# Kernel optimization log

Hardware: AMD Instinct MI355X
Metric: run time of the kernel (lower is better)

The kernel has to match this reference:

```python
import jax, jax.numpy as jnp
import numpy as np

D = 1024       # d_model
H = 16         # nhead
HD = D // H    # head_dim = 64
FF = 4096      # dim_feedforward
EPS = 1e-5


def layer_norm(x, gamma, beta, eps=EPS):
    mu = jnp.mean(x, axis=-1, keepdims=True)
    var = jnp.var(x, axis=-1, keepdims=True)
    return (x - mu) * jax.lax.rsqrt(var + eps) * gamma + beta


def setup_inputs() -> dict:
    key = jax.random.key(0)
    ks = jax.random.split(key, 12)
    rn = lambda k, shape, s=0.02: (jax.random.normal(k, shape, jnp.float32) * s)
    return {
        "src": jax.random.normal(ks[0], (4, 2048, D), jnp.float32),
        "Wqkv": rn(ks[1], (D, 3 * D)),          # qkv_proj weight (bias=False), stored (in,out)
        "Wout": rn(ks[2], (D, D)),              # out_proj weight (bias=False)
        "W1": rn(ks[3], (D, FF)),               # linear1
        "b1": jnp.zeros((FF,), jnp.float32),
        "W2": rn(ks[4], (FF, D)),               # linear2
        "b2": jnp.zeros((D,), jnp.float32),
        "g1": jnp.ones((D,), jnp.float32),      # norm1 weight
        "be1": jnp.zeros((D,), jnp.float32),    # norm1 bias
        "g2": jnp.ones((D,), jnp.float32),      # norm2 weight
        "be2": jnp.zeros((D,), jnp.float32),    # norm2 bias
    }


def reference(src, Wqkv, Wout, W1, b1, W2, b2, g1, be1, g2, be2):
    B, S, _ = src.shape
    # --- self attention (naive/MATH-backend SDPA, post-norm, eval: dropout=0) ---
    qkv = src @ Wqkv                                  # [B,S,3D]
    qkv = qkv.reshape(B, S, 3, H, HD)
    q = qkv[:, :, 0].transpose(0, 2, 1, 3)            # [B,H,S,HD]
    k = qkv[:, :, 1].transpose(0, 2, 1, 3)
    v = qkv[:, :, 2].transpose(0, 2, 1, 3)
    scores = jnp.einsum("bhqd,bhkd->bhqk", q, k) / np.float32(np.sqrt(HD))  # [B,H,S,S]
    attn = jax.nn.softmax(scores, axis=-1)
    ctx = jnp.einsum("bhqk,bhkd->bhqd", attn, v)      # [B,H,S,HD]
    ctx = ctx.transpose(0, 2, 1, 3).reshape(B, S, D)  # [B,S,D]
    attn_out = ctx @ Wout
    # residual + norm1
    x = layer_norm(src + attn_out, g1, be1)
    # --- FFN ---
    ff = jax.nn.relu(x @ W1 + b1) @ W2 + b2
    # residual + norm2
    return layer_norm(x + ff, g2, be2)
```

## Files before the change

### kernel.cpp

```cpp
#include <hip/hip_runtime.h>
#include <hip/hip_bf16.h>


typedef __attribute__((ext_vector_type(8))) short          short8;
typedef __attribute__((ext_vector_type(8))) unsigned short ushort8;
typedef __attribute__((ext_vector_type(4))) float          f32x4;
typedef __attribute__((ext_vector_type(2))) unsigned int   uivec2;

__device__ __forceinline__ unsigned short f2bf(float f) {
    union { float f; unsigned int u; } v; v.f = f;
    unsigned int u = v.u;
    unsigned int r = (u + 0x7fffu + ((u >> 16) & 1u)) >> 16;
    return (unsigned short)r;
}

__device__ __forceinline__ float bf2f(unsigned short u) {
    union { unsigned int u; float f; } v; v.u = ((unsigned int)u) << 16;
    return v.f;
}

__device__ __forceinline__ unsigned int pack_bf16_trunc(float lo, float hi) {
    union { float f; unsigned int u; } a, b; a.f = lo; b.f = hi;
    return __builtin_amdgcn_perm(b.u, a.u, 0x07060302u);
}

__device__ __forceinline__ void async_load16(const void* g, void* l) {
    __builtin_amdgcn_global_load_lds(
        (const __attribute__((address_space(1))) void*)(unsigned long long)g,
        (__attribute__((address_space(3))) void*)(unsigned long long)l,
        16, 0, 0);
}

__global__ __launch_bounds__(256) void cast_bf16_kernel(
    const float* __restrict__ x, unsigned short* __restrict__ y) {
    size_t i = ((size_t)blockIdx.x * 256 + threadIdx.x) * 4;
    float4 v = *(const float4*)(x + i);
    ushort4 o; o.x = f2bf(v.x); o.y = f2bf(v.y); o.z = f2bf(v.z); o.w = f2bf(v.w);
    *(ushort4*)(y + i) = o;
}

__global__ __launch_bounds__(256) void transpose_cast_kernel(
    const float* __restrict__ W, unsigned short* __restrict__ Wt, int K, int N) {
    __shared__ float tile[32][33];
    int n0 = blockIdx.x * 32, k0 = blockIdx.y * 32;
    int tx = threadIdx.x & 31, ty = threadIdx.x >> 5;
#pragma unroll
    for (int i = 0; i < 32; i += 8)
        tile[ty + i][tx] = W[(size_t)(k0 + ty + i) * N + n0 + tx];
    __syncthreads();
#pragma unroll
    for (int i = 0; i < 32; i += 8)
        Wt[(size_t)(n0 + ty + i) * K + k0 + tx] = f2bf(tile[tx][ty + i]);
}

template <int MODE>
__global__ __launch_bounds__(256) void gemm_bf16_kernel(
    const unsigned short* __restrict__ A, const unsigned short* __restrict__ Bt,
    int M, int N, int K, int Kstride,
    float* __restrict__ outF, unsigned short* __restrict__ outB,
    const float* __restrict__ bias,
    const float* __restrict__ resF, const unsigned short* __restrict__ resB,
    unsigned short* __restrict__ vtB) {
    __shared__ unsigned short As[2][128 * 32];
    __shared__ unsigned short Bs[2][128 * 32];

    const int t = threadIdx.x;
    const int m0 = blockIdx.x * 128, n0 = blockIdx.y * 128;
    const int koff = blockIdx.z * K;
    const int wid = t >> 6, lane = t & 63;
    const int wm = wid >> 1, wn = wid & 1;
    const int lr = lane & 15, quad = lane >> 4;

    const int srow = lane >> 2;
    const int sch  = ((lane & 3) ^ (srow & 3)) * 8;
    const unsigned short* Ag =
        A  + (size_t)(m0 + wid * 32 + srow) * Kstride + koff + sch;
    const unsigned short* Bg =
        Bt + (size_t)(n0 + wid * 32 + srow) * Kstride + koff + sch;
    const int wofs = (wid * 32) * 32;
    const size_t rstep = (size_t)16 * Kstride;

    const int axs = ((quad ^ (lr & 3))) * 8;
    f32x4 acc[4][4] = {};

    const int nK = K >> 5;
    async_load16(Ag,         &As[0][wofs]);
    async_load16(Ag + rstep, &As[0][wofs + 16 * 32]);
    async_load16(Bg,         &Bs[0][wofs]);
    async_load16(Bg + rstep, &Bs[0][wofs + 16 * 32]);

    for (int kt = 0; kt < nK; kt++) {
        const int cur = kt & 1, nxt = cur ^ 1;
        __syncthreads();
        if (kt + 1 < nK) {
            const int k1 = (kt + 1) * 32;
            async_load16(Ag + k1,         &As[nxt][wofs]);
            async_load16(Ag + k1 + rstep, &As[nxt][wofs + 16 * 32]);
            async_load16(Bg + k1,         &Bs[nxt][wofs]);
            async_load16(Bg + k1 + rstep, &Bs[nxt][wofs + 16 * 32]);
        }

        short8 af[4], bfr[4];
#pragma unroll
        for (int i = 0; i < 4; i++) {
            af[i]  = *(const short8*)&As[cur][(wm * 64 + i * 16 + lr) * 32 + axs];
            bfr[i] = *(const short8*)&Bs[cur][(wn * 64 + i * 16 + lr) * 32 + axs];
        }
#pragma unroll
        for (int mi = 0; mi < 4; mi++)
#pragma unroll
            for (int ni = 0; ni < 4; ni++)
                acc[mi][ni] = __builtin_amdgcn_mfma_f32_16x16x32_bf16(
                    af[mi], bfr[ni], acc[mi][ni], 0, 0, 0);
    }

    const float QSC = 0.18033688011112042f;
    float* pOut = (MODE == 5) ? outF + (size_t)blockIdx.z * M * N : outF;
#pragma unroll
    for (int mi = 0; mi < 4; mi++)
#pragma unroll
        for (int ni = 0; ni < 4; ni++) {
            const int col  = n0 + wn * 64 + ni * 16 + lr;
            const int row0 = m0 + wm * 64 + mi * 16 + quad * 4;
            if (MODE == 4 && col >= 2048) {
                int bb = row0 >> 11, ss = row0 & 2047, c = col - 2048;
                ushort4 ov;
                ov.x = f2bf(acc[mi][ni][0]); ov.y = f2bf(acc[mi][ni][1]);
                ov.z = f2bf(acc[mi][ni][2]); ov.w = f2bf(acc[mi][ni][3]);
                *(ushort4*)&vtB[((size_t)bb * 1024 + c) * 2048 + ss] = ov;
            } else {
#pragma unroll
                for (int r = 0; r < 4; r++) {
                    size_t idx = (size_t)(row0 + r) * N + col;
                    float v = acc[mi][ni][r];
                    if (MODE == 4) {
                        outB[idx] = f2bf(col < 1024 ? v * QSC : v);
                    } else if (MODE == 0) {
                        outB[idx] = f2bf(v);
                    } else if (MODE == 1) {
                        outF[idx] = v + resF[idx];
                    } else if (MODE == 2) {
                        v += bias[col];
                        outB[idx] = f2bf(v > 0.f ? v : 0.f);
                    } else if (MODE == 3) {
                        outF[idx] = v + bias[col] + bf2f(resB[idx]);
                    } else {
                        pOut[idx] = v;
                    }
                }
            }
        }
}

__global__ __launch_bounds__(256) void attention_kernel(
    const unsigned short* __restrict__ qkv, const unsigned short* __restrict__ Vt,
    unsigned short* __restrict__ ctx) {
    __shared__ unsigned short Kbuf[2][64 * 64];
    __shared__ unsigned short Vbuf[2][64 * 64];

    const int qt = blockIdx.x, h = blockIdx.y, b = blockIdx.z;
    const int t = threadIdx.x, wid = t >> 6, lane = t & 63;
    const int lr = lane & 15, quad = lane >> 4;
    const int q0 = qt * 64 + wid * 16;

    size_t qbase = ((size_t)(b * 2048 + q0 + lr)) * 3072 + h * 64;
    short8 qf0 = *(const short8*)(qkv + qbase + quad * 8);
    short8 qf1 = *(const short8*)(qkv + qbase + 32 + quad * 8);

    const int srow = wid * 8 + (lane >> 3);
    const int sch  = ((lane & 7) ^ (srow & 7)) * 8;
    const unsigned short* Kg =
        qkv + (size_t)b * 2048 * 3072 + 1024 + h * 64 + (size_t)srow * 3072 + sch;
    const unsigned short* Vg =
        Vt + ((size_t)b * 1024 + h * 64 + srow) * 2048 + sch;
    unsigned short* KsB = (unsigned short*)&Kbuf[0][(wid * 8) * 64];
    unsigned short* VsB = (unsigned short*)&Vbuf[0][(wid * 8) * 64];
    const int bufstep = 64 * 64;

    short8 ones;
#pragma unroll
    for (int i = 0; i < 8; i++) ones[i] = (short)0x3F80;

    f32x4 o[4] = {};
    f32x4 lacc = {};

#pragma unroll
    for (int half = 0; half < 2; half++) {
        async_load16(Kg + (size_t)(half * 32) * 3072, KsB + half * 32 * 64);
        async_load16(Vg + (size_t)(half * 32) * 2048, VsB + half * 32 * 64);
    }

    const int swz = lr & 7;

    for (int kt = 0; kt < 32; kt++) {
        const int cur = kt & 1, nxt = cur ^ 1;
        __syncthreads();
        if (kt + 1 < 32) {
#pragma unroll
            for (int half = 0; half < 2; half++) {
                async_load16(Kg + (size_t)((kt + 1) * 64 + half * 32) * 3072,
                             KsB + nxt * bufstep + half * 32 * 64);
                async_load16(Vg + (size_t)(half * 32) * 2048 + (kt + 1) * 64,
                             VsB + nxt * bufstep + half * 32 * 64);
            }
        }

        const unsigned short* Kc = &Kbuf[cur][0];
        const unsigned short* Vc = &Vbuf[cur][0];

        f32x4 s[4] = {};
#pragma unroll
        for (int nt = 0; nt < 4; nt++) {
            const unsigned short* krow = Kc + (nt * 16 + lr) * 64;
            short8 kf0 = *(const short8*)(krow + (quad ^ swz) * 8);
            short8 kf1 = *(const short8*)(krow + ((quad + 4) ^ swz) * 8);
            s[nt] = __builtin_amdgcn_mfma_f32_16x16x32_bf16(kf0, qf0, s[nt], 0, 0, 0);
            s[nt] = __builtin_amdgcn_mfma_f32_16x16x32_bf16(kf1, qf1, s[nt], 0, 0, 0);
        }

        unsigned int aw[4], bw[4];
#pragma unroll
        for (int nt = 0; nt < 4; nt++) {
            float p0 = __builtin_amdgcn_exp2f(s[nt][0]);
            float p1 = __builtin_amdgcn_exp2f(s[nt][1]);
            float p2 = __builtin_amdgcn_exp2f(s[nt][2]);
            float p3 = __builtin_amdgcn_exp2f(s[nt][3]);
            aw[nt] = pack_bf16_trunc(p0, p1);
            bw[nt] = pack_bf16_trunc(p2, p3);
        }

        uivec2 rA = __builtin_amdgcn_permlane32_swap(aw[0], aw[1], false, false);
        uivec2 sA = __builtin_amdgcn_permlane32_swap(aw[2], aw[3], false, false);
        uivec2 rB = __builtin_amdgcn_permlane32_swap(bw[0], bw[1], false, false);
        uivec2 sB = __builtin_amdgcn_permlane32_swap(bw[2], bw[3], false, false);
        uivec2 tA = __builtin_amdgcn_permlane16_swap(rA.x, rA.y, false, false);
        uivec2 uA = __builtin_amdgcn_permlane16_swap(sA.x, sA.y, false, false);
        uivec2 tB = __builtin_amdgcn_permlane16_swap(rB.x, rB.y, false, false);
        uivec2 uB = __builtin_amdgcn_permlane16_swap(sB.x, sB.y, false, false);

        union { unsigned int w[4]; short8 v; } P0, P1;
        P0.w[0] = tA.x; P0.w[1] = tB.x; P0.w[2] = tA.y; P0.w[3] = tB.y;
        P1.w[0] = uA.x; P1.w[1] = uB.x; P1.w[2] = uA.y; P1.w[3] = uB.y;
        short8 pf0 = P0.v;
        short8 pf1 = P1.v;

#pragma unroll
        for (int nt = 0; nt < 4; nt++) {
            const unsigned short* vrow = Vc + (nt * 16 + lr) * 64;
            short8 vf0 = *(const short8*)(vrow + (quad ^ swz) * 8);
            short8 vf1 = *(const short8*)(vrow + ((quad + 4) ^ swz) * 8);
            o[nt] = __builtin_amdgcn_mfma_f32_16x16x32_bf16(pf0, vf0, o[nt], 0, 0, 0);
            o[nt] = __builtin_amdgcn_mfma_f32_16x16x32_bf16(pf1, vf1, o[nt], 0, 0, 0);
        }
        lacc = __builtin_amdgcn_mfma_f32_16x16x32_bf16(pf0, ones, lacc, 0, 0, 0);
        lacc = __builtin_amdgcn_mfma_f32_16x16x32_bf16(pf1, ones, lacc, 0, 0, 0);
    }

#pragma unroll
    for (int r = 0; r < 4; r++) {
        float li = 1.f / lacc[r];
        int q = qt * 64 + wid * 16 + quad * 4 + r;
#pragma unroll
        for (int nt = 0; nt < 4; nt++)
            ctx[((size_t)(b * 2048 + q)) * 1024 + h * 64 + nt * 16 + lr] =
                f2bf(o[nt][r] * li);
    }
}

template <int OUTMODE>
__global__ __launch_bounds__(256) void layernorm_kernel(
    const float* __restrict__ x, const float* __restrict__ g,
    const float* __restrict__ be, float* __restrict__ yF,
    unsigned short* __restrict__ yB) {
    const int row = blockIdx.x, t = threadIdx.x;
    const float* xr = x + (size_t)row * 1024;
    float4 v = *(const float4*)(xr + t * 4);
    float s  = v.x + v.y + v.z + v.w;
    float sq = v.x * v.x + v.y * v.y + v.z * v.z + v.w * v.w;
#pragma unroll
    for (int d = 1; d < 64; d <<= 1) {
        s  += __shfl_xor(s, d, 64);
        sq += __shfl_xor(sq, d, 64);
    }
    __shared__ float sh[8];
    int wid = t >> 6, lane = t & 63;
    if (lane == 0) { sh[wid] = s; sh[4 + wid] = sq; }
    __syncthreads();
    s  = sh[0] + sh[1] + sh[2] + sh[3];
    sq = sh[4] + sh[5] + sh[6] + sh[7];
    float mu  = s * (1.f / 1024.f);
    float var = sq * (1.f / 1024.f) - mu * mu;
    float rstd = rsqrtf(var + 1e-5f);
    float4 gv = *(const float4*)(g + t * 4);
    float4 bv = *(const float4*)(be + t * 4);
    float4 y;
    y.x = (v.x - mu) * rstd * gv.x + bv.x;
    y.y = (v.y - mu) * rstd * gv.y + bv.y;
    y.z = (v.z - mu) * rstd * gv.z + bv.z;
    y.w = (v.w - mu) * rstd * gv.w + bv.w;
    if (OUTMODE == 0) {
        *(float4*)(yF + (size_t)row * 1024 + t * 4) = y;
    } else {
        ushort4 o;
        o.x = f2bf(y.x); o.y = f2bf(y.y); o.z = f2bf(y.z); o.w = f2bf(y.w);
        *(ushort4*)(yB + (size_t)row * 1024 + t * 4) = o;
    }
}

__global__ __launch_bounds__(256) void layernorm_sum2_kernel(
    const float* __restrict__ p0, const float* __restrict__ p1,
    const float* __restrict__ bias, const unsigned short* __restrict__ res,
    const float* __restrict__ g, const float* __restrict__ be,
    float* __restrict__ out) {
    const int row = blockIdx.x, t = threadIdx.x;
    const size_t base = (size_t)row * 1024 + t * 4;
    float4 a = *(const float4*)(p0 + base);
    float4 b = *(const float4*)(p1 + base);
    float4 bi = *(const float4*)(bias + t * 4);
    ushort4 rb = *(const ushort4*)(res + base);
    float4 v;
    v.x = a.x + b.x + bi.x + bf2f(rb.x);
    v.y = a.y + b.y + bi.y + bf2f(rb.y);
    v.z = a.z + b.z + bi.z + bf2f(rb.z);
    v.w = a.w + b.w + bi.w + bf2f(rb.w);
    float s  = v.x + v.y + v.z + v.w;
    float sq = v.x * v.x + v.y * v.y + v.z * v.z + v.w * v.w;
#pragma unroll
    for (int d = 1; d < 64; d <<= 1) {
        s  += __shfl_xor(s, d, 64);
        sq += __shfl_xor(sq, d, 64);
    }
    __shared__ float sh[8];
    int wid = t >> 6, lane = t & 63;
    if (lane == 0) { sh[wid] = s; sh[4 + wid] = sq; }
    __syncthreads();
    s  = sh[0] + sh[1] + sh[2] + sh[3];
    sq = sh[4] + sh[5] + sh[6] + sh[7];
    float mu  = s * (1.f / 1024.f);
    float var = sq * (1.f / 1024.f) - mu * mu;
    float rstd = rsqrtf(var + 1e-5f);
    float4 gv = *(const float4*)(g + t * 4);
    float4 bv = *(const float4*)(be + t * 4);
    float4 y;
    y.x = (v.x - mu) * rstd * gv.x + bv.x;
    y.y = (v.y - mu) * rstd * gv.y + bv.y;
    y.z = (v.z - mu) * rstd * gv.z + bv.z;
    y.w = (v.w - mu) * rstd * gv.w + bv.w;
    *(float4*)(out + base) = y;
}

extern "C" void kernel_launch(void* const* d_in, const int* in_sizes, int n_in,
                              void* d_out, int out_size, void* d_ws, size_t ws_size,
                              hipStream_t stream) {
    const float* src  = (const float*)d_in[0];
    const float* Wqkv = (const float*)d_in[1];
    const float* Wout = (const float*)d_in[2];
    const float* W1   = (const float*)d_in[3];
    const float* b1   = (const float*)d_in[4];
    const float* W2   = (const float*)d_in[5];
    const float* b2   = (const float*)d_in[6];
    const float* g1   = (const float*)d_in[7];
    const float* be1  = (const float*)d_in[8];
    const float* g2   = (const float*)d_in[9];
    const float* be2  = (const float*)d_in[10];
    float* out = (float*)d_out;

    const size_t NT = 8192;
    char* ws = (char*)d_ws;
    unsigned short* src_bf = (unsigned short*)ws; ws += NT * 1024 * 2;
    unsigned short* Wqkv_t = (unsigned short*)ws; ws += (size_t)3072 * 1024 * 2;
    unsigned short* Wout_t = (unsigned short*)ws; ws += (size_t)1024 * 1024 * 2;
    unsigned short* W1_t   = (unsigned short*)ws; ws += (size_t)4096 * 1024 * 2;
    unsigned short* W2_t   = (unsigned short*)ws; ws += (size_t)1024 * 4096 * 2;
    unsigned short* qkv_bf = (unsigned short*)ws; ws += NT * 3072 * 2;
    unsigned short* ctx_bf = (unsigned short*)ws; ws += NT * 1024 * 2;
    float*          x1     = (float*)ws;          ws += NT * 1024 * 4;
    unsigned short* y1_bf  = (unsigned short*)ws; ws += NT * 1024 * 2;
    unsigned short* h_bf   = (unsigned short*)ws; ws += NT * 4096 * 2;
    unsigned short* Vt = h_bf;
    float* part = (float*)qkv_bf;

    cast_bf16_kernel<<<8192, 256, 0, stream>>>(src, src_bf);
    transpose_cast_kernel<<<dim3(96, 32), 256, 0, stream>>>(Wqkv, Wqkv_t, 1024, 3072);
    transpose_cast_kernel<<<dim3(32, 32), 256, 0, stream>>>(Wout, Wout_t, 1024, 1024);
    transpose_cast_kernel<<<dim3(128, 32), 256, 0, stream>>>(W1, W1_t, 1024, 4096);
    transpose_cast_kernel<<<dim3(32, 128), 256, 0, stream>>>(W2, W2_t, 4096, 1024);

    gemm_bf16_kernel<4><<<dim3(64, 24), 256, 0, stream>>>(
        src_bf, Wqkv_t, 8192, 3072, 1024, 1024,
        nullptr, qkv_bf, nullptr, nullptr, nullptr, Vt);
    attention_kernel<<<dim3(32, 16, 4), 256, 0, stream>>>(qkv_bf, Vt, ctx_bf);
    gemm_bf16_kernel<1><<<dim3(64, 8), 256, 0, stream>>>(
        ctx_bf, Wout_t, 8192, 1024, 1024, 1024,
        x1, nullptr, nullptr, src, nullptr, nullptr);
    layernorm_kernel<1><<<8192, 256, 0, stream>>>(x1, g1, be1, nullptr, y1_bf);
    gemm_bf16_kernel<2><<<dim3(64, 32), 256, 0, stream>>>(
        y1_bf, W1_t, 8192, 4096, 1024, 1024,
        nullptr, h_bf, b1, nullptr, nullptr, nullptr);
    gemm_bf16_kernel<5><<<dim3(64, 8, 2), 256, 0, stream>>>(
        h_bf, W2_t, 8192, 1024, 2048, 4096,
        part, nullptr, nullptr, nullptr, nullptr, nullptr);
    layernorm_sum2_kernel<<<8192, 256, 0, stream>>>(
        part, part + NT * 1024, b2, y1_bf, g2, be2, out);
}
```

Before: 520.4 us.

## Add 256x256 tile GEMM kernel with 4-stage async LDS pipeline for QKV/FFN

Adds a new 512-thread GEMM kernel that computes 256x256 output tiles. It uses a 4-slot LDS ring fed by async global-to-LDS loads, with explicit barriers, waitcnt control and raised wave priority around the MFMA bursts so loads overlap compute. The QKV, FF1 and split-K FF2 GEMMs switch to this kernel, while the old 128-tile kernel keeps only the modes that other launches still use. Larger tiles raise data reuse per loaded byte, but they cost 128KB of LDS per block and give fewer blocks, which can leave a partial wave on 256 CUs (for example 384 blocks for QKV).

After: 543.3 us. 4.4% more time.

```diff
diff --git a/kernel.cpp b/kernel.cpp
--- a/kernel.cpp
+++ b/kernel.cpp
@@ -114,14 +114,143 @@
                     af[mi], bfr[ni], acc[mi][ni], 0, 0, 0);
     }
 
-    const float QSC = 0.18033688011112042f;
-    float* pOut = (MODE == 5) ? outF + (size_t)blockIdx.z * M * N : outF;
 #pragma unroll
     for (int mi = 0; mi < 4; mi++)
 #pragma unroll
         for (int ni = 0; ni < 4; ni++) {
             const int col  = n0 + wn * 64 + ni * 16 + lr;
             const int row0 = m0 + wm * 64 + mi * 16 + quad * 4;
+#pragma unroll
+            for (int r = 0; r < 4; r++) {
+                size_t idx = (size_t)(row0 + r) * N + col;
+                float v = acc[mi][ni][r];
+                if (MODE == 0) {
+                    outB[idx] = f2bf(v);
+                } else if (MODE == 1) {
+                    outF[idx] = v + resF[idx];
+                }
+            }
+        }
+}
+
+#define GBAR() do { __builtin_amdgcn_sched_barrier(0); \
+                    __builtin_amdgcn_s_barrier();      \
+                    __builtin_amdgcn_sched_barrier(0); } while (0)
+
+template <int MODE>
+__global__ __launch_bounds__(512, 2) void gemm256_bf16_kernel(
+    const unsigned short* __restrict__ A, const unsigned short* __restrict__ Bt,
+    int M, int N, int K, int Kstride,
+    float* __restrict__ outF, unsigned short* __restrict__ outB,
+    const float* __restrict__ bias,
+    const float* __restrict__ resF, const unsigned short* __restrict__ resB,
+    unsigned short* __restrict__ vtB) {
+    __shared__ unsigned short Alds[4][256 * 32];
+    __shared__ unsigned short Blds[4][256 * 32];
+
+    const int t = threadIdx.x;
+    const int wid = t >> 6, lane = t & 63;
+    const int wm = wid >> 2, wn = wid & 3;
+    const int lr = lane & 15, quad = lane >> 4;
+    const int m0 = blockIdx.x * 256, n0 = blockIdx.y * 256;
+    const int koff = blockIdx.z * K;
+
+    const int srow = wid * 32 + (lane >> 2);
+    const int sch  = ((lane & 3) ^ (srow & 3)) * 8;
+    const unsigned short* Ag = A  + (size_t)(m0 + srow) * Kstride + koff + sch;
+    const unsigned short* Bg = Bt + (size_t)(n0 + srow) * Kstride + koff + sch;
+    const size_t rstep = (size_t)16 * Kstride;
+    unsigned short* AdstW = &Alds[0][(wid * 32) * 32];
+    unsigned short* BdstW = &Blds[0][(wid * 32) * 32];
+
+    const int axs = (quad ^ (lr & 3)) * 8;
+
+    f32x4 acc[8][4] = {};
+    short8 bfr[4];
+
+    const int T = K >> 6;
+    const int Tm2 = T - 2, Tm3 = T - 3;
+
+#define STAGE_A(GP) do { int s_ = (GP) & 3;                                   \
+        const unsigned short* g_ = Ag + (GP) * 32;                            \
+        async_load16(g_,         AdstW + s_ * 256 * 32);                      \
+        async_load16(g_ + rstep, AdstW + s_ * 256 * 32 + 16 * 32); } while (0)
+#define STAGE_B(GP) do { int s_ = (GP) & 3;                                   \
+        const unsigned short* g_ = Bg + (GP) * 32;                            \
+        async_load16(g_,         BdstW + s_ * 256 * 32);                      \
+        async_load16(g_ + rstep, BdstW + s_ * 256 * 32 + 16 * 32); } while (0)
+
+    STAGE_A(0); STAGE_B(0);
+    STAGE_A(1); STAGE_B(1);
+    STAGE_A(2); STAGE_B(2);
+    asm volatile("s_waitcnt vmcnt(4)" ::: "memory");
+    GBAR();
+
+#define GPHASE(SLOT, MB, LOADB)                                               \
+    {                                                                         \
+        short8 af_[4];                                                        \
+        _Pragma("unroll")                                                     \
+        for (int i_ = 0; i_ < 4; i_++)                                        \
+            af_[i_] = *(const short8*)                                        \
+                &Alds[SLOT][(wm * 128 + ((MB) + i_) * 16 + lr) * 32 + axs];   \
+        if (LOADB) {                                                          \
+            _Pragma("unroll")                                                 \
+            for (int i_ = 0; i_ < 4; i_++)                                    \
+                bfr[i_] = *(const short8*)                                    \
+                    &Blds[SLOT][(wn * 64 + i_ * 16 + lr) * 32 + axs];         \
+        }
+
+#define GPHASE_END(MB)                                                        \
+        GBAR();                                                               \
+        asm volatile("s_waitcnt lgkmcnt(0)" ::: "memory");                    \
+        __builtin_amdgcn_sched_barrier(0);                                    \
+        __builtin_amdgcn_s_setprio(1);                                        \
+        _Pragma("unroll")                                                     \
+        for (int mi_ = 0; mi_ < 4; mi_++)                                     \
+            _Pragma("unroll")                                                 \
+            for (int ni_ = 0; ni_ < 4; ni_++)                                 \
+                acc[(MB) + mi_][ni_] = __builtin_amdgcn_mfma_f32_16x16x32_bf16( \
+                    af_[mi_], bfr[ni_], acc[(MB) + mi_][ni_], 0, 0, 0);       \
+        __builtin_amdgcn_s_setprio(0);                                        \
+        GBAR();                                                               \
+    }
+
+    for (int t2 = 0; t2 < T; t2++) {
+        const int s0 = (2 * t2) & 3, s1 = (2 * t2 + 1) & 3;
+        const int gA = 2 * t2 + 3, gB = 2 * t2 + 4;
+
+        GPHASE(s0, 0, 1)
+            if (t2 <= Tm2) STAGE_A(gA);
+        GPHASE_END(0)
+        GPHASE(s0, 4, 0)
+            if (t2 <= Tm2) STAGE_B(gA);
+        GPHASE_END(4)
+        GPHASE(s1, 0, 1)
+            if (t2 <= Tm3) STAGE_A(gB);
+        GPHASE_END(0)
+        GPHASE(s1, 4, 0)
+            if (t2 <= Tm3) STAGE_B(gB);
+            if (t2 == Tm2) {
+                asm volatile("s_waitcnt vmcnt(0)" ::: "memory");
+            } else if (t2 < Tm2) {
+                asm volatile("s_waitcnt vmcnt(4)" ::: "memory");
+            }
+        GPHASE_END(4)
+    }
+
+#undef GPHASE
+#undef GPHASE_END
+#undef STAGE_A
+#undef STAGE_B
+
+    const float QSC = 0.18033688011112042f;
+    float* pOut = (MODE == 5) ? outF + (size_t)blockIdx.z * M * N : outF;
+#pragma unroll
+    for (int mi = 0; mi < 8; mi++)
+#pragma unroll
+        for (int ni = 0; ni < 4; ni++) {
+            const int col  = n0 + wn * 64 + ni * 16 + lr;
+            const int row0 = m0 + wm * 128 + mi * 16 + quad * 4;
             if (MODE == 4 && col >= 2048) {
                 int bb = row0 >> 11, ss = row0 & 2047, c = col - 2048;
                 ushort4 ov;
@@ -135,16 +264,10 @@
                     float v = acc[mi][ni][r];
                     if (MODE == 4) {
                         outB[idx] = f2bf(col < 1024 ? v * QSC : v);
-                    } else if (MODE == 0) {
-                        outB[idx] = f2bf(v);
-                    } else if (MODE == 1) {
-                        outF[idx] = v + resF[idx];
                     } else if (MODE == 2) {
                         v += bias[col];
                         outB[idx] = f2bf(v > 0.f ? v : 0.f);
-                    } else if (MODE == 3) {
-                        outF[idx] = v + bias[col] + bf2f(resB[idx]);
-                    } else {
+                    } else if (MODE == 5) {
                         pOut[idx] = v;
                     }
                 }
@@ -386,7 +509,7 @@
     transpose_cast_kernel<<<dim3(128, 32), 256, 0, stream>>>(W1, W1_t, 1024, 4096);
     transpose_cast_kernel<<<dim3(32, 128), 256, 0, stream>>>(W2, W2_t, 4096, 1024);
 
-    gemm_bf16_kernel<4><<<dim3(64, 24), 256, 0, stream>>>(
+    gemm256_bf16_kernel<4><<<dim3(32, 12), 512, 0, stream>>>(
         src_bf, Wqkv_t, 8192, 3072, 1024, 1024,
         nullptr, qkv_bf, nullptr, nullptr, nullptr, Vt);
     attention_kernel<<<dim3(32, 16, 4), 256, 0, stream>>>(qkv_bf, Vt, ctx_bf);
@@ -394,10 +517,10 @@
         ctx_bf, Wout_t, 8192, 1024, 1024, 1024,
         x1, nullptr, nullptr, src, nullptr, nullptr);
     layernorm_kernel<1><<<8192, 256, 0, stream>>>(x1, g1, be1, nullptr, y1_bf);
-    gemm_bf16_kernel<2><<<dim3(64, 32), 256, 0, stream>>>(
+    gemm256_bf16_kernel<2><<<dim3(32, 16), 512, 0, stream>>>(
         y1_bf, W1_t, 8192, 4096, 1024, 1024,
         nullptr, h_bf, b1, nullptr, nullptr, nullptr);
-    gemm_bf16_kernel<5><<<dim3(64, 8, 2), 256, 0, stream>>>(
+    gemm256_bf16_kernel<5><<<dim3(32, 4, 2), 512, 0, stream>>>(
         h_bf, W2_t, 8192, 1024, 2048, 4096,
         part, nullptr, nullptr, nullptr, nullptr, nullptr);
     layernorm_sum2_kernel<<<8192, 256, 0, stream>>>(
```
